# Optimization experiments

Measured on AMD Instinct MI355X. Metric: run time of the kernel, lower is better.

## Reference

```python
import jax, jax.numpy as jnp
import numpy as np

N_NODES = 100000
NEG_SLOPE = 0.2  # DGL GATConv default


def gat_layer(x, W, al, ar, src, dst):
    # x: [N, F_in], W: [F_in, H*D], al/ar: [H, D]
    H, D = al.shape
    f = (x @ W).reshape(-1, H, D)                      # [N, H, D]
    el = jnp.einsum('nhd,hd->nh', f, al)               # src attn term
    er = jnp.einsum('nhd,hd->nh', f, ar)               # dst attn term
    e = jax.nn.leaky_relu(el[src] + er[dst], NEG_SLOPE)  # [E, H]
    # segment softmax over incoming edges of each dst node
    m = jax.ops.segment_max(e, dst, num_segments=N_NODES)
    m = jnp.where(jnp.isfinite(m), m, jnp.zeros_like(m))  # isolated nodes -> -inf guard
    ex = jnp.exp(e - m[dst])                           # [E, H]
    s = jax.ops.segment_sum(ex, dst, num_segments=N_NODES)
    alpha = ex / (s[dst] + 1e-9)                       # [E, H]
    msg = f[src] * alpha[:, :, None]                   # [E, H, D]
    out = jax.ops.segment_sum(msg, dst, num_segments=N_NODES)  # [N, H, D]
    return out.reshape(N_NODES, H * D)


def setup_inputs() -> dict:
    key = jax.random.key(0)
    ks = jax.random.split(key, 12)
    x = jax.random.normal(ks[0], (N_NODES, 128), dtype=jnp.float32)
    edge_index = jax.random.randint(ks[1], (2, 1600000), 0, N_NODES, dtype=jnp.int32)
    sc = 0.05
    W0 = jax.random.normal(ks[2], (128, 128), dtype=jnp.float32) * sc
    al0 = jax.random.normal(ks[3], (4, 32), dtype=jnp.float32) * sc
    ar0 = jax.random.normal(ks[4], (4, 32), dtype=jnp.float32) * sc
    W1 = jax.random.normal(ks[5], (128, 128), dtype=jnp.float32) * sc
    al1 = jax.random.normal(ks[6], (4, 32), dtype=jnp.float32) * sc
    ar1 = jax.random.normal(ks[7], (4, 32), dtype=jnp.float32) * sc
    W2 = jax.random.normal(ks[8], (128, 128), dtype=jnp.float32) * sc
    al2 = jax.random.normal(ks[9], (4, 32), dtype=jnp.float32) * sc
    ar2 = jax.random.normal(ks[10], (4, 32), dtype=jnp.float32) * sc
    return {"x": x, "edge_index": edge_index,
            "W0": W0, "al0": al0, "ar0": ar0,
            "W1": W1, "al1": al1, "ar1": ar1,
            "W2": W2, "al2": al2, "ar2": ar2}


def reference(x, edge_index, W0, al0, ar0, W1, al1, ar1, W2, al2, ar2):
    src, dst = edge_index[0], edge_index[1]
    h = x
    for (W, al, ar) in ((W0, al0, ar0), (W1, al1, ar1), (W2, al2, ar2)):
        h = gat_layer(h, W, al, ar, src, dst)
        h = jax.nn.relu(h)  # dropout_rate = 0.0 -> identity
    return h
```

## Files before the change

### kernel.cpp

```cpp
#include <hip/hip_runtime.h>
#include <math.h>

#define NEG_SLOPE 0.2f
#define NBUCK 512
#define BHCHUNK 8192
#define BCHUNK 4096

typedef __attribute__((ext_vector_type(8))) short short8;
typedef __attribute__((ext_vector_type(4))) float f32x4;

__device__ __forceinline__ unsigned short bf16rne(float x) {
    unsigned u = __float_as_uint(x);
    u += 0x7fffu + ((u >> 16) & 1u);
    return (unsigned short)(u >> 16);
}
__device__ __forceinline__ unsigned pack_bf2(float x, float y) {
    unsigned ux = __float_as_uint(x), uy = __float_as_uint(y);
    ux = (ux + 0x7fffu + ((ux >> 16) & 1u)) >> 16;
    uy = (uy + 0x7fffu + ((uy >> 16) & 1u)) & 0xffff0000u;
    return ux | uy;
}

__global__ __launch_bounds__(256) void k_front(
    const int* __restrict__ dst, int* __restrict__ bcnt, int E,
    const float4* __restrict__ x, uint4* __restrict__ Xb, int n8,
    const float* __restrict__ w0, const float* __restrict__ w1,
    const float* __restrict__ w2, unsigned short* __restrict__ Wt,
    int nbB, int nbCvt) {
    __shared__ int cnt[NBUCK];
    int bb = blockIdx.x, t = threadIdx.x;
    if (bb < nbB) {
        for (int i = t; i < NBUCK; i += 256) cnt[i] = 0;
        __syncthreads();
        int e0 = bb * BHCHUNK;
        int n = min(BHCHUNK, E - e0);
        for (int i = t; i < n; i += 256) atomicAdd(&cnt[dst[e0 + i] >> 8], 1);
        __syncthreads();
        for (int i = t; i < NBUCK; i += 256)
            if (cnt[i]) atomicAdd(&bcnt[i], cnt[i]);
    } else if (bb < nbB + nbCvt) {
        int id = (bb - nbB) * 256 + t;
        if (id < n8) {
            float4 a = x[id * 2], b = x[id * 2 + 1];
            uint4 o;
            o.x = pack_bf2(a.x, a.y);
            o.y = pack_bf2(a.z, a.w);
            o.z = pack_bf2(b.x, b.y);
            o.w = pack_bf2(b.z, b.w);
            Xb[id] = o;
        }
    } else {
        int id = (bb - nbB - nbCvt) * 256 + t;
        int layer = id >> 14, rem = id & 16383;
        int k = rem >> 7, n = rem & 127;
        const float* W = (layer == 0) ? w0 : (layer == 1) ? w1 : w2;
        Wt[layer * 16384 + n * 128 + k] = bf16rne(W[k * 128 + n]);
    }
}

__global__ void k_bscan(const int* __restrict__ bcnt, int* __restrict__ bbase,
                        int* __restrict__ bcur, int* __restrict__ rowstart,
                        int N, int E) {
    __shared__ int sd[NBUCK];
    int t = threadIdx.x;
    int c = bcnt[t];
    sd[t] = c;
    __syncthreads();
    for (int s = 1; s < NBUCK; s <<= 1) {
        int x = (t >= s) ? sd[t - s] : 0;
        __syncthreads();
        sd[t] += x;
        __syncthreads();
    }
    int excl = sd[t] - c;
    bbase[t] = excl;
    bcur[t] = excl;
    if (t == NBUCK - 1) bbase[NBUCK] = excl + c;
    if (t == 0) rowstart[N] = E;
}

__global__ __launch_bounds__(256) void k_bin(
    const int* __restrict__ src, const int* __restrict__ dst,
    int* __restrict__ bcur, unsigned* __restrict__ packed, int E) {
    __shared__ int cnt[NBUCK];
    __shared__ int gbase[NBUCK];
    for (int i = threadIdx.x; i < NBUCK; i += 256) cnt[i] = 0;
    __syncthreads();
    int e0 = blockIdx.x * BCHUNK;
    int n = min(BCHUNK, E - e0);
    for (int i = threadIdx.x; i < n; i += 256)
        atomicAdd(&cnt[dst[e0 + i] >> 8], 1);
    __syncthreads();
    for (int i = threadIdx.x; i < NBUCK; i += 256) {
        int c = cnt[i];
        gbase[i] = c ? atomicAdd(&bcur[i], c) : 0;
        cnt[i] = 0;
    }
    __syncthreads();
    for (int i = threadIdx.x; i < n; i += 256) {
        int d = dst[e0 + i];
        int b = d >> 8;
        int o = atomicAdd(&cnt[b], 1);
        packed[gbase[b] + o] = ((unsigned)src[e0 + i] << 8) | (unsigned)(d & 255);
    }
}

__global__ __launch_bounds__(256) void k_place2(
    const unsigned* __restrict__ packed, const int* __restrict__ bbase,
    int* __restrict__ rowstart, unsigned* __restrict__ cpack, int N) {
    __shared__ int cnt[256], sd[256], lcur[256];
    int b = blockIdx.x, t = threadIdx.x;
    int base = bbase[b], end = bbase[b + 1];
    cnt[t] = 0;
    __syncthreads();
    for (int i = base + t; i < end; i += 256)
        atomicAdd(&cnt[packed[i] & 255u], 1);
    __syncthreads();
    sd[t] = cnt[t];
    __syncthreads();
    for (int s = 1; s < 256; s <<= 1) {
        int x = (t >= s) ? sd[t - s] : 0;
        __syncthreads();
        sd[t] += x;
        __syncthreads();
    }
    int excl = sd[t] - cnt[t];
    int gid = (b << 8) + t;
    if (gid < N) rowstart[gid] = base + excl;
    lcur[t] = base + excl;
    __syncthreads();
    for (int i = base + t; i < end; i += 256) {
        unsigned p = packed[i];
        unsigned dl = p & 255u;
        int pos = atomicAdd(&lcur[dl], 1);
        cpack[pos] = (dl << 17) | (p >> 8);
    }
}

__global__ __launch_bounds__(256) void k_gemm(
    const unsigned short* __restrict__ Ab,
    const unsigned short* __restrict__ Wt,
    const float* __restrict__ alv, const float* __restrict__ arv,
    unsigned short* __restrict__ Fb,
    float* __restrict__ el, float* __restrict__ er, int M) {
    __shared__ unsigned short wls[128][136];
    int t = threadIdx.x;
    int wv = t >> 6, l = t & 63;
    int l15 = l & 15, quad = l >> 4;
    int row0 = blockIdx.x * 128 + wv * 32;

    union U { uint4 u; short8 s; };

    int rA0 = min(row0 + l15, M - 1);
    int rA1 = min(row0 + 16 + l15, M - 1);
    const uint4* pA0 = (const uint4*)(Ab + (size_t)rA0 * 128) + quad;
    const uint4* pA1 = (const uint4*)(Ab + (size_t)rA1 * 128) + quad;
    U A0[4], A1[4];
#pragma unroll
    for (int ks = 0; ks < 4; ks++) {
        A0[ks].u = pA0[ks * 4];
        A1[ks].u = pA1[ks * 4];
    }

    {
        const uint4* gw = (const uint4*)Wt;
        uint4 wtmp[8];
#pragma unroll
        for (int it = 0; it < 8; it++) wtmp[it] = gw[it * 256 + t];
#pragma unroll
        for (int it = 0; it < 8; it++) {
            int flat = it * 256 + t;
            int r = flat >> 4, c = flat & 15;
            *(uint4*)&wls[r][c * 8] = wtmp[it];
        }
    }
    __syncthreads();

    f32x4 acc[2][8];
#pragma unroll
    for (int mi = 0; mi < 2; mi++)
#pragma unroll
        for (int nt = 0; nt < 8; nt++)
            acc[mi][nt] = (f32x4){0.f, 0.f, 0.f, 0.f};

#pragma unroll
    for (int ks = 0; ks < 4; ks++) {
        U b[8];
#pragma unroll
        for (int nt = 0; nt < 8; nt++)
            b[nt].u = *(const uint4*)&wls[nt * 16 + l15][(quad + ks * 4) * 8];
#pragma unroll
        for (int nt = 0; nt < 8; nt++) {
            acc[0][nt] = __builtin_amdgcn_mfma_f32_16x16x32_bf16(A0[ks].s, b[nt].s, acc[0][nt], 0, 0, 0);
            acc[1][nt] = __builtin_amdgcn_mfma_f32_16x16x32_bf16(A1[ks].s, b[nt].s, acc[1][nt], 0, 0, 0);
        }
    }

    __syncthreads();
    unsigned short (*cst)[136] = (unsigned short (*)[136])&wls[wv * 32][0];

#pragma unroll
    for (int mi = 0; mi < 2; mi++)
#pragma unroll
        for (int nt = 0; nt < 8; nt++)
#pragma unroll
            for (int r = 0; r < 4; r++)
                cst[mi * 16 + quad * 4 + r][nt * 16 + l15] = bf16rne(acc[mi][nt][r]);

    int rrow = l >> 1;
    int cb = (l & 1) * 64;
    int grow = row0 + rrow;
    bool ok = grow < M;
    float pe[2] = {0.f, 0.f}, pr[2] = {0.f, 0.f};
#pragma unroll
    for (int i = 0; i < 8; i++) {
        uint4 v = *(const uint4*)&cst[rrow][cb + i * 8];
        if (ok) ((uint4*)(Fb + (size_t)grow * 128 + cb))[i] = v;
        int hi = i >> 2;
        int c0 = cb + i * 8;
        unsigned uu[4] = {v.x, v.y, v.z, v.w};
#pragma unroll
        for (int q = 0; q < 4; q++) {
            float fa = __uint_as_float(uu[q] << 16);
            float fb = __uint_as_float(uu[q] & 0xffff0000u);
            pe[hi] += fa * alv[c0 + 2 * q] + fb * alv[c0 + 2 * q + 1];
            pr[hi] += fa * arv[c0 + 2 * q] + fb * arv[c0 + 2 * q + 1];
        }
    }
    float qe0 = __shfl_xor(pe[0], 1, 64), qe1 = __shfl_xor(pe[1], 1, 64);
    float qr0 = __shfl_xor(pr[0], 1, 64), qr1 = __shfl_xor(pr[1], 1, 64);
    if (((l & 1) == 0) && ok) {
        *(float4*)&el[(size_t)grow * 4] = make_float4(pe[0], pe[1], qe0, qe1);
        *(float4*)&er[(size_t)grow * 4] = make_float4(pr[0], pr[1], qr0, qr1);
    }
}

template <int OUT_BF16>
__global__ __launch_bounds__(256) void k_aggr(
    const int* __restrict__ rowstart, const unsigned* __restrict__ cpack,
    const float* __restrict__ el, const float* __restrict__ er,
    const uint4* __restrict__ F4, void* __restrict__ outp, int N, int E) {
    int lane = threadIdx.x & 63;
    int sub = lane >> 4;
    int l16 = lane & 15;
    int h = l16 >> 2;
    int w = blockIdx.x * 16 + ((threadIdx.x >> 6) << 2) + sub;
    bool active = w < N;
    int wc = active ? w : N - 1;
    int start = rowstart[wc];
    int dg = active ? (rowstart[wc + 1] - start) : 0;
    float rr = er[(size_t)wc * 4 + h];

    float s_acc = 0.f;
    float a0 = 0.f, a1 = 0.f, a2 = 0.f, a3 = 0.f;
    float a4 = 0.f, a5 = 0.f, a6 = 0.f, a7 = 0.f;

    int ncc = (dg + 3) >> 2;
    int m = max(ncc, __shfl_xor(ncc, 16, 64));
    int nccmax = max(m, __shfl_xor(m, 32, 64));
    int full = dg >> 2;
    int mf = min(full, __shfl_xor(full, 16, 64));
    int minfull = min(mf, __shfl_xor(mf, 32, 64));

    auto loadc = [&](int c, uint4* fb, float* eb) {
        int j = c << 2;
        if (c < minfull) {
#pragma unroll
            for (int u = 0; u < 4; u++) {
                int e = start + j + u;
                int s = (int)(cpack[e] & 0x1ffffu);
                fb[u] = F4[(size_t)s * 16 + l16];
                eb[u] = el[(size_t)s * 4 + h];
            }
        } else {
#pragma unroll
            for (int u = 0; u < 4; u++) {
                int jj = j + u;
                int e = min(max(start + min(jj, dg - 1), 0), E - 1);
                int s = (int)(cpack[e] & 0x1ffffu);
                fb[u] = F4[(size_t)s * 16 + l16];
                float ev = el[(size_t)s * 4 + h];
                eb[u] = (jj < dg) ? ev : -1e30f;
            }
        }
    };
    auto consume = [&](const uint4* fb, const float* eb) {
#pragma unroll
        for (int u = 0; u < 4; u++) {
            float e = eb[u] + rr;
            e = fmaxf(e, NEG_SLOPE * e);
            float p = __expf(e);
            s_acc += p;
            a0 += p * __uint_as_float(fb[u].x << 16);
            a1 += p * __uint_as_float(fb[u].x & 0xffff0000u);
            a2 += p * __uint_as_float(fb[u].y << 16);
            a3 += p * __uint_as_float(fb[u].y & 0xffff0000u);
            a4 += p * __uint_as_float(fb[u].z << 16);
            a5 += p * __uint_as_float(fb[u].z & 0xffff0000u);
            a6 += p * __uint_as_float(fb[u].w << 16);
            a7 += p * __uint_as_float(fb[u].w & 0xffff0000u);
        }
    };

    uint4 f0[4], f1[4];
    float e0[4], e1[4];
    if (nccmax > 0) {
        loadc(0, f0, e0);
        for (int c = 1; c < nccmax; c++) {
            if (c & 1) { loadc(c, f1, e1); consume(f0, e0); }
            else       { loadc(c, f0, e0); consume(f1, e1); }
        }
        if (nccmax & 1) consume(f0, e0); else consume(f1, e1);
    }

    if (!active) return;
    float inv = 1.f / (s_acc + 1e-9f);
    a0 = fmaxf(a0 * inv, 0.f); a1 = fmaxf(a1 * inv, 0.f);
    a2 = fmaxf(a2 * inv, 0.f); a3 = fmaxf(a3 * inv, 0.f);
    a4 = fmaxf(a4 * inv, 0.f); a5 = fmaxf(a5 * inv, 0.f);
    a6 = fmaxf(a6 * inv, 0.f); a7 = fmaxf(a7 * inv, 0.f);
    if (OUT_BF16) {
        uint4 pk;
        pk.x = pack_bf2(a0, a1);
        pk.y = pack_bf2(a2, a3);
        pk.z = pack_bf2(a4, a5);
        pk.w = pack_bf2(a6, a7);
        ((uint4*)outp)[(size_t)w * 16 + l16] = pk;
    } else {
        float4* op = (float4*)outp + (size_t)w * 32 + l16 * 2;
        op[0] = make_float4(a0, a1, a2, a3);
        op[1] = make_float4(a4, a5, a6, a7);
    }
}


extern "C" void kernel_launch(void* const* d_in, const int* in_sizes, int n_in,
                              void* d_out, int out_size, void* d_ws, size_t ws_size,
                              hipStream_t stream) {
    const float* x = (const float*)d_in[0];
    const int* ei = (const int*)d_in[1];
    int N = in_sizes[0] / 128;
    int E = in_sizes[1] / 2;
    const int* src = ei;
    const int* dst = ei + E;
    const float* Wm[3] = {(const float*)d_in[2], (const float*)d_in[5], (const float*)d_in[8]};
    const float* al[3] = {(const float*)d_in[3], (const float*)d_in[6], (const float*)d_in[9]};
    const float* ar[3] = {(const float*)d_in[4], (const float*)d_in[7], (const float*)d_in[10]};

    char* p = (char*)d_ws;
    auto carve = [&](size_t bytes) {
        char* r = p;
        p += (bytes + 255) & ~(size_t)255;
        return r;
    };
    unsigned short* Xb = (unsigned short*)carve((size_t)N * 128 * 2);
    unsigned short* Hb = (unsigned short*)carve((size_t)N * 128 * 2);
    unsigned short* Fb = (unsigned short*)carve((size_t)N * 128 * 2);
    unsigned short* Wt = (unsigned short*)carve((size_t)3 * 16384 * 2);
    float* el       = (float*)carve((size_t)N * 4 * 4);
    float* er       = (float*)carve((size_t)N * 4 * 4);
    int* rowstart   = (int*)carve((size_t)(N + 1) * 4);
    unsigned* cpack = (unsigned*)carve((size_t)E * 4);
    unsigned* packed= (unsigned*)carve((size_t)E * 4);
    int* bcnt       = (int*)carve((size_t)NBUCK * 4);
    int* bbase      = (int*)carve((size_t)(NBUCK + 1) * 4);
    int* bcur       = (int*)carve((size_t)NBUCK * 4);

    int NBUSED = (N + 255) >> 8;

    hipMemsetAsync(bcnt, 0, NBUCK * 4, stream);
    int nbB = (E + BHCHUNK - 1) / BHCHUNK;
    int n8 = N * 128 / 8;
    int nbCvt = (n8 + 255) / 256;
    int nbPrep = (3 * 16384) / 256;
    k_front<<<nbB + nbCvt + nbPrep, 256, 0, stream>>>(
        dst, bcnt, E, (const float4*)x, (uint4*)Xb, n8,
        Wm[0], Wm[1], Wm[2], Wt, nbB, nbCvt);
    k_bscan<<<1, NBUCK, 0, stream>>>(bcnt, bbase, bcur, rowstart, N, E);
    k_bin<<<(E + BCHUNK - 1) / BCHUNK, 256, 0, stream>>>(src, dst, bcur, packed, E);
    k_place2<<<NBUSED, 256, 0, stream>>>(packed, bbase, rowstart, cpack, N);

    int gb = (N + 127) / 128;
    int ab = (N + 15) / 16;
    k_gemm<<<gb, 256, 0, stream>>>(Xb, Wt, al[0], ar[0], Fb, el, er, N);
    k_aggr<1><<<ab, 256, 0, stream>>>(rowstart, cpack, el, er, (const uint4*)Fb, Hb, N, E);

    k_gemm<<<gb, 256, 0, stream>>>(Hb, Wt + 16384, al[1], ar[1], Fb, el, er, N);
    k_aggr<1><<<ab, 256, 0, stream>>>(rowstart, cpack, el, er, (const uint4*)Fb, Hb, N, E);

    k_gemm<<<gb, 256, 0, stream>>>(Hb, Wt + 32768, al[2], ar[2], Fb, el, er, N);
    k_aggr<0><<<ab, 256, 0, stream>>>(rowstart, cpack, el, er, (const uint4*)Fb, d_out, N, E);
}
```

Measured before the change: 468.3 us.

## Fuse CSR build and input conversion into one cooperative grid-sync kernel

Replaces the memset and four separate preprocessing kernels (front histogram and convert, bucket scan, binning, placement) with a single cooperative kernel of 512 blocks that uses grid.sync between phases. The aim is to remove per-launch overheads and the idle gaps between small dependent kernels. In exchange, each phase now runs on a fixed, smaller grid with grid-stride loops, and the grid barriers add cost. The x and W conversion no longer overlaps with the histogram phase.

```diff
diff --git a/kernel.cpp b/kernel.cpp
--- a/kernel.cpp
+++ b/kernel.cpp
@@ -1,10 +1,14 @@
 #include <hip/hip_runtime.h>
+#include <hip/hip_cooperative_groups.h>
 #include <math.h>
 
 #define NEG_SLOPE 0.2f
 #define NBUCK 512
 #define BHCHUNK 8192
 #define BCHUNK 4096
+#define CSRBLK 512
+
+namespace cg = cooperative_groups;
 
 typedef __attribute__((ext_vector_type(8))) short short8;
 typedef __attribute__((ext_vector_type(4))) float f32x4;
@@ -21,119 +25,135 @@
     return ux | uy;
 }
 
-__global__ __launch_bounds__(256) void k_front(
-    const int* __restrict__ dst, int* __restrict__ bcnt, int E,
+__global__ __launch_bounds__(256) void k_csr(
+    const int* __restrict__ src, const int* __restrict__ dst, int E,
     const float4* __restrict__ x, uint4* __restrict__ Xb, int n8,
     const float* __restrict__ w0, const float* __restrict__ w1,
     const float* __restrict__ w2, unsigned short* __restrict__ Wt,
-    int nbB, int nbCvt) {
-    __shared__ int cnt[NBUCK];
-    int bb = blockIdx.x, t = threadIdx.x;
-    if (bb < nbB) {
-        for (int i = t; i < NBUCK; i += 256) cnt[i] = 0;
-        __syncthreads();
-        int e0 = bb * BHCHUNK;
-        int n = min(BHCHUNK, E - e0);
-        for (int i = t; i < n; i += 256) atomicAdd(&cnt[dst[e0 + i] >> 8], 1);
-        __syncthreads();
-        for (int i = t; i < NBUCK; i += 256)
-            if (cnt[i]) atomicAdd(&bcnt[i], cnt[i]);
-    } else if (bb < nbB + nbCvt) {
-        int id = (bb - nbB) * 256 + t;
-        if (id < n8) {
-            float4 a = x[id * 2], b = x[id * 2 + 1];
-            uint4 o;
-            o.x = pack_bf2(a.x, a.y);
-            o.y = pack_bf2(a.z, a.w);
-            o.z = pack_bf2(b.x, b.y);
-            o.w = pack_bf2(b.z, b.w);
-            Xb[id] = o;
-        }
-    } else {
-        int id = (bb - nbB - nbCvt) * 256 + t;
+    int* __restrict__ bcnt, int* __restrict__ bbase, int* __restrict__ bcur,
+    int* __restrict__ rowstart, unsigned* __restrict__ packed,
+    unsigned* __restrict__ cpack, int N) {
+    cg::grid_group grid = cg::this_grid();
+    __shared__ int sm[1024];
+    int t = threadIdx.x;
+    int gtid = blockIdx.x * 256 + t;
+    int nth = gridDim.x * 256;
+
+    if (blockIdx.x == 0)
+        for (int i = t; i < NBUCK; i += 256) bcnt[i] = 0;
+    for (int id = gtid; id < n8; id += nth) {
+        float4 a = x[id * 2], b = x[id * 2 + 1];
+        uint4 o;
+        o.x = pack_bf2(a.x, a.y);
+        o.y = pack_bf2(a.z, a.w);
+        o.z = pack_bf2(b.x, b.y);
+        o.w = pack_bf2(b.z, b.w);
+        Xb[id] = o;
+    }
+    for (int id = gtid; id < 3 * 16384; id += nth) {
         int layer = id >> 14, rem = id & 16383;
         int k = rem >> 7, n = rem & 127;
         const float* W = (layer == 0) ? w0 : (layer == 1) ? w1 : w2;
         Wt[layer * 16384 + n * 128 + k] = bf16rne(W[k * 128 + n]);
     }
-}
-
-__global__ void k_bscan(const int* __restrict__ bcnt, int* __restrict__ bbase,
-                        int* __restrict__ bcur, int* __restrict__ rowstart,
-                        int N, int E) {
-    __shared__ int sd[NBUCK];
-    int t = threadIdx.x;
-    int c = bcnt[t];
-    sd[t] = c;
-    __syncthreads();
-    for (int s = 1; s < NBUCK; s <<= 1) {
-        int x = (t >= s) ? sd[t - s] : 0;
-        __syncthreads();
-        sd[t] += x;
-        __syncthreads();
-    }
-    int excl = sd[t] - c;
-    bbase[t] = excl;
-    bcur[t] = excl;
-    if (t == NBUCK - 1) bbase[NBUCK] = excl + c;
-    if (t == 0) rowstart[N] = E;
-}
-
-__global__ __launch_bounds__(256) void k_bin(
-    const int* __restrict__ src, const int* __restrict__ dst,
-    int* __restrict__ bcur, unsigned* __restrict__ packed, int E) {
-    __shared__ int cnt[NBUCK];
-    __shared__ int gbase[NBUCK];
-    for (int i = threadIdx.x; i < NBUCK; i += 256) cnt[i] = 0;
-    __syncthreads();
-    int e0 = blockIdx.x * BCHUNK;
-    int n = min(BCHUNK, E - e0);
-    for (int i = threadIdx.x; i < n; i += 256)
-        atomicAdd(&cnt[dst[e0 + i] >> 8], 1);
-    __syncthreads();
-    for (int i = threadIdx.x; i < NBUCK; i += 256) {
-        int c = cnt[i];
-        gbase[i] = c ? atomicAdd(&bcur[i], c) : 0;
-        cnt[i] = 0;
-    }
-    __syncthreads();
-    for (int i = threadIdx.x; i < n; i += 256) {
-        int d = dst[e0 + i];
-        int b = d >> 8;
-        int o = atomicAdd(&cnt[b], 1);
-        packed[gbase[b] + o] = ((unsigned)src[e0 + i] << 8) | (unsigned)(d & 255);
-    }
-}
-
-__global__ __launch_bounds__(256) void k_place2(
-    const unsigned* __restrict__ packed, const int* __restrict__ bbase,
-    int* __restrict__ rowstart, unsigned* __restrict__ cpack, int N) {
-    __shared__ int cnt[256], sd[256], lcur[256];
-    int b = blockIdx.x, t = threadIdx.x;
-    int base = bbase[b], end = bbase[b + 1];
-    cnt[t] = 0;
-    __syncthreads();
-    for (int i = base + t; i < end; i += 256)
-        atomicAdd(&cnt[packed[i] & 255u], 1);
-    __syncthreads();
-    sd[t] = cnt[t];
-    __syncthreads();
-    for (int s = 1; s < 256; s <<= 1) {
-        int x = (t >= s) ? sd[t - s] : 0;
-        __syncthreads();
-        sd[t] += x;
-        __syncthreads();
-    }
-    int excl = sd[t] - cnt[t];
-    int gid = (b << 8) + t;
-    if (gid < N) rowstart[gid] = base + excl;
-    lcur[t] = base + excl;
-    __syncthreads();
-    for (int i = base + t; i < end; i += 256) {
-        unsigned p = packed[i];
-        unsigned dl = p & 255u;
-        int pos = atomicAdd(&lcur[dl], 1);
-        cpack[pos] = (dl << 17) | (p >> 8);
+    __threadfence();
+    grid.sync();
+
+    int nbB = (E + BHCHUNK - 1) / BHCHUNK;
+    for (int bb = blockIdx.x; bb < nbB; bb += gridDim.x) {
+        for (int i = t; i < NBUCK; i += 256) sm[i] = 0;
+        __syncthreads();
+        int e0 = bb * BHCHUNK;
+        int n = min(BHCHUNK, E - e0);
+        for (int i = t; i < n; i += 256) atomicAdd(&sm[dst[e0 + i] >> 8], 1);
+        __syncthreads();
+        for (int i = t; i < NBUCK; i += 256)
+            if (sm[i]) atomicAdd(&bcnt[i], sm[i]);
+        __syncthreads();
+    }
+    __threadfence();
+    grid.sync();
+
+    if (blockIdx.x == 0) {
+        sm[t] = bcnt[t];
+        sm[t + 256] = bcnt[t + 256];
+        __syncthreads();
+        for (int s = 1; s < NBUCK; s <<= 1) {
+            int a0 = (t >= s) ? sm[t - s] : 0;
+            int a1 = (t + 256 >= s) ? sm[t + 256 - s] : 0;
+            __syncthreads();
+            sm[t] += a0;
+            sm[t + 256] += a1;
+            __syncthreads();
+        }
+        bbase[t] = sm[t] - bcnt[t];
+        bbase[t + 256] = sm[t + 256] - bcnt[t + 256];
+        bcur[t] = bbase[t];
+        bcur[t + 256] = bbase[t + 256];
+        if (t == 0) { bbase[NBUCK] = E; rowstart[N] = E; }
+        __threadfence();
+    }
+    grid.sync();
+
+    int nch = (E + BCHUNK - 1) / BCHUNK;
+    int* cnt = sm;
+    int* gbase = sm + NBUCK;
+    for (int ch = blockIdx.x; ch < nch; ch += gridDim.x) {
+        for (int i = t; i < NBUCK; i += 256) cnt[i] = 0;
+        __syncthreads();
+        int e0 = ch * BCHUNK;
+        int n = min(BCHUNK, E - e0);
+        for (int i = t; i < n; i += 256)
+            atomicAdd(&cnt[dst[e0 + i] >> 8], 1);
+        __syncthreads();
+        for (int i = t; i < NBUCK; i += 256) {
+            int c = cnt[i];
+            gbase[i] = c ? atomicAdd(&bcur[i], c) : 0;
+            cnt[i] = 0;
+        }
+        __syncthreads();
+        for (int i = t; i < n; i += 256) {
+            int d = dst[e0 + i];
+            int b = d >> 8;
+            int o = atomicAdd(&cnt[b], 1);
+            packed[gbase[b] + o] = ((unsigned)src[e0 + i] << 8) | (unsigned)(d & 255);
+        }
+        __syncthreads();
+    }
+    __threadfence();
+    grid.sync();
+
+    int NB = (N + 255) >> 8;
+    int* c2 = sm;
+    int* s2 = sm + 256;
+    int* lc = sm + 512;
+    for (int b = blockIdx.x; b < NB; b += gridDim.x) {
+        int base = bbase[b], end = bbase[b + 1];
+        c2[t] = 0;
+        __syncthreads();
+        for (int i = base + t; i < end; i += 256)
+            atomicAdd(&c2[packed[i] & 255u], 1);
+        __syncthreads();
+        s2[t] = c2[t];
+        __syncthreads();
+        for (int s = 1; s < 256; s <<= 1) {
+            int xv = (t >= s) ? s2[t - s] : 0;
+            __syncthreads();
+            s2[t] += xv;
+            __syncthreads();
+        }
+        int excl = s2[t] - c2[t];
+        int gid = (b << 8) + t;
+        if (gid < N) rowstart[gid] = base + excl;
+        lc[t] = base + excl;
+        __syncthreads();
+        for (int i = base + t; i < end; i += 256) {
+            unsigned p = packed[i];
+            unsigned dl = p & 255u;
+            int pos = atomicAdd(&lc[dl], 1);
+            cpack[pos] = (dl << 17) | (p >> 8);
+        }
+        __syncthreads();
     }
 }
 
@@ -366,19 +386,22 @@
     int* bbase      = (int*)carve((size_t)(NBUCK + 1) * 4);
     int* bcur       = (int*)carve((size_t)NBUCK * 4);
 
-    int NBUSED = (N + 255) >> 8;
-
-    hipMemsetAsync(bcnt, 0, NBUCK * 4, stream);
-    int nbB = (E + BHCHUNK - 1) / BHCHUNK;
     int n8 = N * 128 / 8;
-    int nbCvt = (n8 + 255) / 256;
-    int nbPrep = (3 * 16384) / 256;
-    k_front<<<nbB + nbCvt + nbPrep, 256, 0, stream>>>(
-        dst, bcnt, E, (const float4*)x, (uint4*)Xb, n8,
-        Wm[0], Wm[1], Wm[2], Wt, nbB, nbCvt);
-    k_bscan<<<1, NBUCK, 0, stream>>>(bcnt, bbase, bcur, rowstart, N, E);
-    k_bin<<<(E + BCHUNK - 1) / BCHUNK, 256, 0, stream>>>(src, dst, bcur, packed, E);
-    k_place2<<<NBUSED, 256, 0, stream>>>(packed, bbase, rowstart, cpack, N);
+    {
+        const int* a_src = src; const int* a_dst = dst; int a_E = E;
+        const float4* a_x = (const float4*)x; uint4* a_Xb = (uint4*)Xb; int a_n8 = n8;
+        const float* a_w0 = Wm[0]; const float* a_w1 = Wm[1]; const float* a_w2 = Wm[2];
+        unsigned short* a_Wt = Wt;
+        int* a_bcnt = bcnt; int* a_bbase = bbase; int* a_bcur = bcur;
+        int* a_rowstart = rowstart; unsigned* a_packed = packed;
+        unsigned* a_cpack = cpack; int a_N = N;
+        void* args[] = {&a_src, &a_dst, &a_E, &a_x, &a_Xb, &a_n8,
+                        &a_w0, &a_w1, &a_w2, &a_Wt,
+                        &a_bcnt, &a_bbase, &a_bcur, &a_rowstart,
+                        &a_packed, &a_cpack, &a_N};
+        hipLaunchCooperativeKernel((const void*)k_csr, dim3(CSRBLK), dim3(256),
+                                   args, 0, stream);
+    }
 
     int gb = (N + 127) / 128;
     int ab = (N + 15) / 16;
```

Measured after the change: 855.0 us. +82.6%, slower.
